# Optimization experiments

Hardware: AMD Instinct MI355X
Metric: run time of the kernel (lower is better)

The kernel has to match this reference:

```python
import jax, jax.numpy as jnp
import numpy as np

B, N, DIN, D, HID, C, K = 16, 1024, 768, 512, 128, 20, 64
H = W = 32
EPS = 1e-5  # BatchNorm eps (inference mode with running stats)


def _conv(x, w, pad=0, dil=1):
    return jax.lax.conv_general_dilated(
        x, w, (1, 1), [(pad, pad), (pad, pad)],
        rhs_dilation=(dil, dil),
        dimension_numbers=('NCHW', 'OIHW', 'NCHW'))


def _bn(x, g, b, m, v):
    inv = jax.lax.rsqrt(v + EPS)
    return (x - m[None, :, None, None]) * (g * inv)[None, :, None, None] + b[None, :, None, None]


def _l2norm(x):
    n = jnp.sqrt(jnp.sum(x * x, axis=-1, keepdims=True))
    return x / jnp.maximum(n, 1e-12)  # matches F.normalize(eps=1e-12)


def setup_inputs():
    key = jax.random.key(0)
    ks = jax.random.split(key, 12)

    def conv_w(k, o, i, kh, kw):
        return jax.random.normal(k, (o, i, kh, kw), jnp.float32) / np.sqrt(i * kh * kw)

    def bn_p(k, c):
        k1, k2 = jax.random.split(k)
        return (jnp.ones(c, jnp.float32), jnp.zeros(c, jnp.float32),
                0.1 * jax.random.normal(k1, (c,), jnp.float32),
                jax.random.uniform(k2, (c,), jnp.float32, 0.5, 1.5))

    g0, b0, m0, v0 = bn_p(ks[3], D)
    gr, br, mr, vr = bn_p(ks[4], HID)
    gl, bl, ml, vl = bn_p(ks[5], HID)
    gg, bg, mg, vg = bn_p(ks[6], HID)
    gp, bp, mp, vp = bn_p(ks[7], D)
    return {
        'patch_feats': jax.random.normal(ks[0], (B, N, DIN), jnp.float32),
        'protos': _l2norm(jax.random.normal(ks[1], (C, K, D), jnp.float32)),  # hybrid protos, L2-normed as in __init__
        'w0': conv_w(ks[2], D, DIN, 1, 1), 'g0': g0, 'b0': b0, 'm0': m0, 'v0': v0,
        'wr': conv_w(ks[8], HID, D, 1, 1), 'gr': gr, 'br': br, 'mr': mr, 'vr': vr,
        'wl': conv_w(ks[9], HID, HID, 3, 3), 'gl': gl, 'bl': bl, 'ml': ml, 'vl': vl,
        'wg': conv_w(ks[10], HID, HID, 3, 3), 'gg': gg, 'bg': bg, 'mg': mg, 'vg': vg,
        'wp': conv_w(ks[11], D, 2 * HID, 1, 1), 'gp': gp, 'bp': bp, 'mp': mp, 'vp': vp,
        'wf': conv_w(jax.random.fold_in(key, 99), D, D, 1, 1),
        'bf': jnp.zeros(D, jnp.float32),
        'logit_scale': jnp.float32(10.0),
    }


def reference(patch_feats, protos, w0, g0, b0, m0, v0, wr, gr, br, mr, vr,
              wl, gl, bl, ml, vl, wg, gg, bg, mg, vg, wp, gp, bp, mp, vp,
              wf, bf, logit_scale):
    Bq, Nq, Din = patch_feats.shape
    x = patch_feats.transpose(0, 2, 1).reshape(Bq, Din, H, W)
    # adapter: 1x1 conv -> BN -> ReLU
    x = jax.nn.relu(_bn(_conv(x, w0), g0, b0, m0, v0))
    # ResidualContextBlock
    res = x
    o = jax.nn.relu(_bn(_conv(x, wr), gr, br, mr, vr))
    l = jax.nn.relu(_bn(_conv(o, wl, pad=1), gl, bl, ml, vl))
    g = jax.nn.relu(_bn(_conv(o, wg, pad=2, dil=2), gg, bg, mg, vg))
    o = _bn(_conv(jnp.concatenate([l, g], axis=1), wp), gp, bp, mp, vp)
    x = jax.nn.relu(o + res)
    # final 1x1 conv (with bias)
    x = _conv(x, wf) + bf[None, :, None, None]
    # back to [B, N, D], L2 normalize
    x = x.reshape(Bq, D, Nq).transpose(0, 2, 1)
    x = _l2norm(x)
    # per-class cosine sims + double max reduction (vectorized over classes)
    sims = jnp.einsum('bnd,ckd->bcnk', x, protos)  # [B,C,N,K]
    A = sims.max(axis=-1)                          # [B,C,N] patch->proto max
    act_maps = A.reshape(Bq, C, H, W)
    logits = A.max(axis=-1) * logit_scale          # [B,C]
    return logits, act_maps, x
```

## Files before the change

kernel.cpp:

```cpp
#include <hip/hip_runtime.h>
#include <math.h>

#define BN_EPS 1e-5f

typedef __attribute__((ext_vector_type(8))) short short8v;
typedef __attribute__((ext_vector_type(8))) unsigned short ushort8v;
typedef __attribute__((ext_vector_type(4))) float f32x4;

__device__ __forceinline__ unsigned short f2b(float f) {
    unsigned int u = __float_as_uint(f);
    return (unsigned short)((u + 0x7FFFu + ((u >> 16) & 1u)) >> 16);
}
__device__ __forceinline__ float b2f(unsigned short h) {
    return __uint_as_float(((unsigned int)h) << 16);
}

__global__ __launch_bounds__(256) void f2b_kernel(
    const float* __restrict__ in, unsigned short* __restrict__ out, int n8)
{
    int i = blockIdx.x * 256 + threadIdx.x;
    if (i >= n8) return;
    const float4* p = (const float4*)(in + (size_t)i * 8);
    float4 a = p[0], b = p[1];
    ushort8v r;
    r[0] = f2b(a.x); r[1] = f2b(a.y); r[2] = f2b(a.z); r[3] = f2b(a.w);
    r[4] = f2b(b.x); r[5] = f2b(b.y); r[6] = f2b(b.z); r[7] = f2b(b.w);
    *(ushort8v*)(out + (size_t)i * 8) = r;
}

__global__ __launch_bounds__(256) void convw_kernel(
    const float* __restrict__ wl, const float* __restrict__ wg,
    unsigned short* __restrict__ out)
{
    int i = blockIdx.x * 256 + threadIdx.x;
    if (i >= 294912) return;
    int br = i >= 147456;
    int j  = i - br * 147456;
    int tap = j >> 14, oc = (j >> 7) & 127, ic = j & 127;
    const float* src = br ? wg : wl;
    out[i] = f2b(src[((oc << 7) + ic) * 9 + tap]);
}

__global__ __launch_bounds__(256) void zero_kernel(unsigned short* __restrict__ p, int n8)
{
    int i = blockIdx.x * 256 + threadIdx.x;
    if (i >= n8) return;
    ushort8v z;
#pragma unroll
    for (int k = 0; k < 8; ++k) z[k] = 0;
    *(ushort8v*)(p + (size_t)i * 8) = z;
}

template <int EPI>
__global__ __launch_bounds__(256) void mfma_gemm(
    const unsigned short* __restrict__ A, int lda,
    const unsigned short* __restrict__ Wt, int ldw,
    void* __restrict__ outp, int ldc, int Kdim,
    const float* __restrict__ bng, const float* __restrict__ bnb,
    const float* __restrict__ bnm, const float* __restrict__ bnv,
    const unsigned short* __restrict__ res, int ldres,
    const float* __restrict__ bias)
{
    __shared__ short8v Asta[512];
    __shared__ short8v Bsta[512];
    const int t  = threadIdx.x;
    const int l  = t & 63, w = t >> 6;
    const int wm = w >> 1, wn = w & 1;
    const int m0 = blockIdx.x << 7, n0 = blockIdx.y << 7;

    const int r0  = t & 127;
    const int kb0 = t >> 7;

    const unsigned short* Ap = A  + (size_t)(m0 + r0) * lda + kb0 * 8;
    const unsigned short* Bp = Wt + (size_t)(n0 + r0) * ldw + kb0 * 8;

    f32x4 acc[4][4];
#pragma unroll
    for (int mf = 0; mf < 4; ++mf)
#pragma unroll
        for (int nf = 0; nf < 4; ++nf)
#pragma unroll
            for (int j = 0; j < 4; ++j) acc[mf][nf][j] = 0.f;

    const int arow = wm * 64 + (l & 15);
    const int brow = wn * 64 + (l & 15);
    const int kq   = l >> 4;

    for (int k0 = 0; k0 < Kdim; k0 += 32) {
        short8v a0 = *(const short8v*)(Ap + k0);
        short8v a1 = *(const short8v*)(Ap + k0 + 16);
        short8v b0 = *(const short8v*)(Bp + k0);
        short8v b1 = *(const short8v*)(Bp + k0 + 16);
        __syncthreads();
        Asta[kb0 * 128 + r0]       = a0;
        Asta[(kb0 + 2) * 128 + r0] = a1;
        Bsta[kb0 * 128 + r0]       = b0;
        Bsta[(kb0 + 2) * 128 + r0] = b1;
        __syncthreads();
        short8v af[4], bfv[4];
#pragma unroll
        for (int mf = 0; mf < 4; ++mf) af[mf]  = Asta[kq * 128 + arow + mf * 16];
#pragma unroll
        for (int nf = 0; nf < 4; ++nf) bfv[nf] = Bsta[kq * 128 + brow + nf * 16];
#pragma unroll
        for (int mf = 0; mf < 4; ++mf)
#pragma unroll
            for (int nf = 0; nf < 4; ++nf)
                acc[mf][nf] = __builtin_amdgcn_mfma_f32_16x16x32_bf16(
                    af[mf], bfv[nf], acc[mf][nf], 0, 0, 0);
    }

    float s[4], sh[4];
    int cols[4];
#pragma unroll
    for (int nf = 0; nf < 4; ++nf) {
        int col = n0 + wn * 64 + nf * 16 + (l & 15);
        cols[nf] = col;
        if (EPI == 2) { s[nf] = 1.f; sh[nf] = bias[col]; }
        else {
            float sc = bng[col] * rsqrtf(bnv[col] + BN_EPS);
            s[nf]  = sc;
            sh[nf] = bnb[col] - bnm[col] * sc;
        }
    }
#pragma unroll
    for (int mf = 0; mf < 4; ++mf) {
#pragma unroll
        for (int j = 0; j < 4; ++j) {
            int row = m0 + wm * 64 + mf * 16 + kq * 4 + j;
#pragma unroll
            for (int nf = 0; nf < 4; ++nf) {
                float v = acc[mf][nf][j] * s[nf] + sh[nf];
                if (EPI == 1) v += b2f(res[(size_t)row * ldres + cols[nf]]);
                if (EPI != 2) v = fmaxf(v, 0.f);
                if (EPI == 2) {
                    ((float*)outp)[(size_t)row * ldc + cols[nf]] = v;
                } else if (EPI == 3) {
                    int b = row >> 10, h = (row >> 5) & 31, ww = row & 31;
                    size_t pidx = ((size_t)(b * 36 + h + 2) * 36 + (ww + 2)) * 128 + cols[nf];
                    ((unsigned short*)outp)[pidx] = f2b(v);
                } else {
                    ((unsigned short*)outp)[(size_t)row * ldc + cols[nf]] = f2b(v);
                }
            }
        }
    }
}

__global__ __launch_bounds__(256) void conv_mfma(
    const unsigned short* __restrict__ opad,
    const unsigned short* __restrict__ wt_all,
    const float* __restrict__ g1, const float* __restrict__ b1,
    const float* __restrict__ m1, const float* __restrict__ v1,
    const float* __restrict__ g2, const float* __restrict__ b2,
    const float* __restrict__ m2, const float* __restrict__ v2,
    unsigned short* __restrict__ lg)
{
    __shared__ short8v Asta[512];
    __shared__ short8v Bsta[512];
    const int t  = threadIdx.x;
    const int l  = t & 63, w = t >> 6;
    const int wm = w >> 1, wn = w & 1;
    const int m0 = blockIdx.x << 7;
    const int br = blockIdx.y;
    const int dil = 1 + br;
    const unsigned short* wtb = wt_all + (size_t)br * 147456;

    const int r0  = t & 127;
    const int kb0 = t >> 7;
    const int m   = m0 + r0;
    const int bb  = m >> 10, h = (m >> 5) & 31, wc = m & 31;
    const ptrdiff_t pbase = ((ptrdiff_t)(bb * 36 + h + 2) * 36 + (wc + 2)) * 128;

    f32x4 acc[4][4];
#pragma unroll
    for (int mf = 0; mf < 4; ++mf)
#pragma unroll
        for (int nf = 0; nf < 4; ++nf)
#pragma unroll
            for (int j = 0; j < 4; ++j) acc[mf][nf][j] = 0.f;

    const int arow = wm * 64 + (l & 15);
    const int brow = wn * 64 + (l & 15);
    const int kq   = l >> 4;

    for (int tap = 0; tap < 9; ++tap) {
        const int dh = tap / 3 - 1, dw = tap % 3 - 1;
        const unsigned short* Ap  = opad + pbase + (ptrdiff_t)((dh * 36 + dw) * dil) * 128 + kb0 * 8;
        const unsigned short* Bpt = wtb + (size_t)tap * 16384 + (size_t)r0 * 128 + kb0 * 8;
#pragma unroll
        for (int k0 = 0; k0 < 128; k0 += 32) {
            short8v a0 = *(const short8v*)(Ap + k0);
            short8v a1 = *(const short8v*)(Ap + k0 + 16);
            short8v b0 = *(const short8v*)(Bpt + k0);
            short8v b1 = *(const short8v*)(Bpt + k0 + 16);
            __syncthreads();
            Asta[kb0 * 128 + r0]       = a0;
            Asta[(kb0 + 2) * 128 + r0] = a1;
            Bsta[kb0 * 128 + r0]       = b0;
            Bsta[(kb0 + 2) * 128 + r0] = b1;
            __syncthreads();
            short8v af[4], bfv[4];
#pragma unroll
            for (int mf = 0; mf < 4; ++mf) af[mf]  = Asta[kq * 128 + arow + mf * 16];
#pragma unroll
            for (int nf = 0; nf < 4; ++nf) bfv[nf] = Bsta[kq * 128 + brow + nf * 16];
#pragma unroll
            for (int mf = 0; mf < 4; ++mf)
#pragma unroll
                for (int nf = 0; nf < 4; ++nf)
                    acc[mf][nf] = __builtin_amdgcn_mfma_f32_16x16x32_bf16(
                        af[mf], bfv[nf], acc[mf][nf], 0, 0, 0);
        }
    }

    const float* gg = br ? g2 : g1;
    const float* gb = br ? b2 : b1;
    const float* gm = br ? m2 : m1;
    const float* gv = br ? v2 : v1;
    float s[4], sh[4];
    int cols[4];
#pragma unroll
    for (int nf = 0; nf < 4; ++nf) {
        int col = wn * 64 + nf * 16 + (l & 15);
        cols[nf] = col;
        float sc = gg[col] * rsqrtf(gv[col] + BN_EPS);
        s[nf]  = sc;
        sh[nf] = gb[col] - gm[col] * sc;
    }
#pragma unroll
    for (int mf = 0; mf < 4; ++mf) {
#pragma unroll
        for (int j = 0; j < 4; ++j) {
            int row = m0 + wm * 64 + mf * 16 + kq * 4 + j;
#pragma unroll
            for (int nf = 0; nf < 4; ++nf) {
                float v = fmaxf(acc[mf][nf][j] * s[nf] + sh[nf], 0.f);
                lg[(size_t)row * 256 + br * 128 + cols[nf]] = f2b(v);
            }
        }
    }
}

__global__ __launch_bounds__(256) void l2norm_rows(
    float* __restrict__ x, unsigned short* __restrict__ xn)
{
    const int t    = threadIdx.x;
    const int wv   = t >> 6, lane = t & 63;
    const int row  = (blockIdx.x << 2) + wv;
    float* p = x + (size_t)row * 512 + (lane << 3);
    float4 a = *(float4*)p;
    float4 b = *(float4*)(p + 4);
    float ss = a.x * a.x + a.y * a.y + a.z * a.z + a.w * a.w +
               b.x * b.x + b.y * b.y + b.z * b.z + b.w * b.w;
#pragma unroll
    for (int off = 32; off >= 1; off >>= 1) ss += __shfl_xor(ss, off);
    float sc = 1.f / fmaxf(sqrtf(ss), 1e-12f);
    a.x *= sc; a.y *= sc; a.z *= sc; a.w *= sc;
    b.x *= sc; b.y *= sc; b.z *= sc; b.w *= sc;
    *(float4*)p       = a;
    *(float4*)(p + 4) = b;
    ushort8v r;
    r[0] = f2b(a.x); r[1] = f2b(a.y); r[2] = f2b(a.z); r[3] = f2b(a.w);
    r[4] = f2b(b.x); r[5] = f2b(b.y); r[6] = f2b(b.z); r[7] = f2b(b.w);
    *(ushort8v*)(xn + (size_t)row * 512 + (lane << 3)) = r;
}

__global__ __launch_bounds__(256) void sims_mfma(
    const unsigned short* __restrict__ xn,
    const unsigned short* __restrict__ protos,
    float* __restrict__ act)
{
    __shared__ short8v Asta[512];
    __shared__ short8v Bsta[256];
    const int t = threadIdx.x;
    const int l = t & 63, w = t >> 6;
    const int m0 = blockIdx.x << 7;
    const int c  = blockIdx.y;

    const int r0  = t & 127, kb0 = t >> 7;
    const int rb  = t & 63,  kbb = t >> 6;
    const unsigned short* Ap = xn + (size_t)(m0 + r0) * 512 + kb0 * 8;
    const unsigned short* Bp = protos + ((size_t)c * 64 + rb) * 512 + kbb * 8;

    f32x4 acc[2][4];
#pragma unroll
    for (int mf = 0; mf < 2; ++mf)
#pragma unroll
        for (int nf = 0; nf < 4; ++nf)
#pragma unroll
            for (int j = 0; j < 4; ++j) acc[mf][nf][j] = 0.f;

    const int arow = w * 32 + (l & 15);
    const int brow = l & 15;
    const int kq   = l >> 4;

    for (int k0 = 0; k0 < 512; k0 += 32) {
        short8v a0 = *(const short8v*)(Ap + k0);
        short8v a1 = *(const short8v*)(Ap + k0 + 16);
        short8v b0 = *(const short8v*)(Bp + k0);
        __syncthreads();
        Asta[kb0 * 128 + r0]       = a0;
        Asta[(kb0 + 2) * 128 + r0] = a1;
        Bsta[kbb * 64 + rb]        = b0;
        __syncthreads();
        short8v af[2], bfv[4];
        af[0] = Asta[kq * 128 + arow];
        af[1] = Asta[kq * 128 + arow + 16];
#pragma unroll
        for (int nf = 0; nf < 4; ++nf) bfv[nf] = Bsta[kq * 64 + brow + nf * 16];
#pragma unroll
        for (int mf = 0; mf < 2; ++mf)
#pragma unroll
            for (int nf = 0; nf < 4; ++nf)
                acc[mf][nf] = __builtin_amdgcn_mfma_f32_16x16x32_bf16(
                    af[mf], bfv[nf], acc[mf][nf], 0, 0, 0);
    }

#pragma unroll
    for (int mf = 0; mf < 2; ++mf) {
        float vj[4];
#pragma unroll
        for (int j = 0; j < 4; ++j) {
            float v = fmaxf(fmaxf(acc[mf][0][j], acc[mf][1][j]),
                            fmaxf(acc[mf][2][j], acc[mf][3][j]));
            v = fmaxf(v, __shfl_xor(v, 1));
            v = fmaxf(v, __shfl_xor(v, 2));
            v = fmaxf(v, __shfl_xor(v, 4));
            v = fmaxf(v, __shfl_xor(v, 8));
            vj[j] = v;
        }
        if ((l & 15) == 0) {
            int rowb = m0 + w * 32 + mf * 16 + kq * 4;
#pragma unroll
            for (int j = 0; j < 4; ++j) {
                int row = rowb + j;
                int bb = row >> 10, n = row & 1023;
                act[(((size_t)(bb * 20 + c)) << 10) + n] = vj[j];
            }
        }
    }
}

__global__ __launch_bounds__(256) void logits_max(
    const float* __restrict__ act, const float* __restrict__ lsc,
    float* __restrict__ logits)
{
    const int bc = blockIdx.x;
    const int t  = threadIdx.x;
    float4 v = *(const float4*)(act + ((size_t)bc << 10) + (t << 2));
    float mx = fmaxf(fmaxf(v.x, v.y), fmaxf(v.z, v.w));
#pragma unroll
    for (int off = 32; off >= 1; off >>= 1) mx = fmaxf(mx, __shfl_xor(mx, off));
    __shared__ float wm[4];
    if ((t & 63) == 0) wm[t >> 6] = mx;
    __syncthreads();
    if (t == 0) {
        float m2 = fmaxf(fmaxf(wm[0], wm[1]), fmaxf(wm[2], wm[3]));
        logits[bc] = m2 * lsc[0];
    }
}

extern "C" void kernel_launch(void* const* d_in, const int* in_sizes, int n_in,
                              void* d_out, int out_size, void* d_ws, size_t ws_size,
                              hipStream_t stream)
{
    const float* pf   = (const float*)d_in[0];
    const float* prot = (const float*)d_in[1];
    const float* w0   = (const float*)d_in[2];
    const float* g0   = (const float*)d_in[3];
    const float* b0   = (const float*)d_in[4];
    const float* m0v  = (const float*)d_in[5];
    const float* v0   = (const float*)d_in[6];
    const float* wr   = (const float*)d_in[7];
    const float* gr   = (const float*)d_in[8];
    const float* br   = (const float*)d_in[9];
    const float* mr   = (const float*)d_in[10];
    const float* vr   = (const float*)d_in[11];
    const float* wl   = (const float*)d_in[12];
    const float* gl   = (const float*)d_in[13];
    const float* bl   = (const float*)d_in[14];
    const float* ml   = (const float*)d_in[15];
    const float* vl   = (const float*)d_in[16];
    const float* wg   = (const float*)d_in[17];
    const float* gG   = (const float*)d_in[18];
    const float* bG   = (const float*)d_in[19];
    const float* mG   = (const float*)d_in[20];
    const float* vG   = (const float*)d_in[21];
    const float* wp   = (const float*)d_in[22];
    const float* gp   = (const float*)d_in[23];
    const float* bp   = (const float*)d_in[24];
    const float* mp   = (const float*)d_in[25];
    const float* vp   = (const float*)d_in[26];
    const float* wf   = (const float*)d_in[27];
    const float* bf_  = (const float*)d_in[28];
    const float* lsc  = (const float*)d_in[29];

    char* ws = (char*)d_ws;
    unsigned short* pf_bf    = (unsigned short*)(ws);
    unsigned short* w0_bf    = (unsigned short*)(ws + 25165824);
    unsigned short* wr_bf    = (unsigned short*)(ws + 25952256);
    unsigned short* wt_bf    = (unsigned short*)(ws + 26083328);
    unsigned short* wp_bf    = (unsigned short*)(ws + 26673152);
    unsigned short* wf_bf    = (unsigned short*)(ws + 26935296);
    unsigned short* prot_bf  = (unsigned short*)(ws + 27459584);
    unsigned short* x1_bf    = (unsigned short*)(ws + 28770304);
    unsigned short* opad     = (unsigned short*)(ws + 45547520);
    unsigned short* lg_bf    = (unsigned short*)(ws + 50855936);
    unsigned short* x2_bf    = (unsigned short*)(ws + 59244544);
    unsigned short* xn_bf    = (unsigned short*)(ws + 76021760);

    float* out    = (float*)d_out;
    float* logits = out;
    float* act    = out + 320;
    float* xo     = out + 328000;

    f2b_kernel<<<6144, 256, 0, stream>>>(pf,   pf_bf,   1572864);
    f2b_kernel<<<192,  256, 0, stream>>>(w0,   w0_bf,   49152);
    f2b_kernel<<<32,   256, 0, stream>>>(wr,   wr_bf,   8192);
    f2b_kernel<<<64,   256, 0, stream>>>(wp,   wp_bf,   16384);
    f2b_kernel<<<128,  256, 0, stream>>>(wf,   wf_bf,   32768);
    f2b_kernel<<<320,  256, 0, stream>>>(prot, prot_bf, 81920);
    convw_kernel<<<1152, 256, 0, stream>>>(wl, wg, wt_bf);
    zero_kernel<<<1296, 256, 0, stream>>>(opad, 331776);

    mfma_gemm<0><<<dim3(128, 4), 256, 0, stream>>>(
        pf_bf, 768, w0_bf, 768, x1_bf, 512, 768,
        g0, b0, m0v, v0, nullptr, 0, nullptr);

    mfma_gemm<3><<<dim3(128, 1), 256, 0, stream>>>(
        x1_bf, 512, wr_bf, 512, opad, 0, 512,
        gr, br, mr, vr, nullptr, 0, nullptr);

    conv_mfma<<<dim3(128, 2), 256, 0, stream>>>(
        opad, wt_bf, gl, bl, ml, vl, gG, bG, mG, vG, lg_bf);

    mfma_gemm<1><<<dim3(128, 4), 256, 0, stream>>>(
        lg_bf, 256, wp_bf, 256, x2_bf, 512, 256,
        gp, bp, mp, vp, x1_bf, 512, nullptr);

    mfma_gemm<2><<<dim3(128, 4), 256, 0, stream>>>(
        x2_bf, 512, wf_bf, 512, xo, 512, 512,
        nullptr, nullptr, nullptr, nullptr, nullptr, 0, bf_);

    l2norm_rows<<<4096, 256, 0, stream>>>(xo, xn_bf);

    sims_mfma<<<dim3(128, 20), 256, 0, stream>>>(xn_bf, prot_bf, act);

    logits_max<<<320, 256, 0, stream>>>(act, lsc, logits);
}
```

Measured before the change: 226.9 us.

## Retile dilated conv and sims kernels, batch weight conversions into one launch

The five small weight fp32-to-bf16 conversion launches are merged into a single kernel that dispatches by index range. The 3x3 conv kernel now uses 64-row tiles and stages a full 128-wide K slice per tap, so there are two barriers per tap instead of eight, and twice as many blocks are launched. The similarity kernel now covers two classes (128 prototypes) per block with a 4x4 MFMA tile per wave, so each loaded activation tile is reused across more prototypes and half as many blocks are launched. The trade-offs are more LDS per conv block and lower occupancy or parallelism in the sims kernel.

```diff
diff --git a/kernel.cpp b/kernel.cpp
--- a/kernel.cpp
+++ b/kernel.cpp
@@ -26,6 +26,30 @@
     r[0] = f2b(a.x); r[1] = f2b(a.y); r[2] = f2b(a.z); r[3] = f2b(a.w);
     r[4] = f2b(b.x); r[5] = f2b(b.y); r[6] = f2b(b.z); r[7] = f2b(b.w);
     *(ushort8v*)(out + (size_t)i * 8) = r;
+}
+
+__global__ __launch_bounds__(256) void f2b_multi(
+    const float* __restrict__ w0, const float* __restrict__ wr,
+    const float* __restrict__ wp, const float* __restrict__ wf,
+    const float* __restrict__ prot,
+    unsigned short* __restrict__ w0o, unsigned short* __restrict__ wro,
+    unsigned short* __restrict__ wpo, unsigned short* __restrict__ wfo,
+    unsigned short* __restrict__ proto)
+{
+    int i = blockIdx.x * 256 + threadIdx.x;
+    const float* src; unsigned short* dst; int off;
+    if      (i <  49152) { src = w0;   dst = w0o;   off = i; }
+    else if (i <  57344) { src = wr;   dst = wro;   off = i - 49152; }
+    else if (i <  73728) { src = wp;   dst = wpo;   off = i - 57344; }
+    else if (i < 106496) { src = wf;   dst = wfo;   off = i - 73728; }
+    else if (i < 188416) { src = prot; dst = proto; off = i - 106496; }
+    else return;
+    const float4* p = (const float4*)(src + (size_t)off * 8);
+    float4 a = p[0], b = p[1];
+    ushort8v r;
+    r[0] = f2b(a.x); r[1] = f2b(a.y); r[2] = f2b(a.z); r[3] = f2b(a.w);
+    r[4] = f2b(b.x); r[5] = f2b(b.y); r[6] = f2b(b.z); r[7] = f2b(b.w);
+    *(ushort8v*)(dst + (size_t)off * 8) = r;
 }
 
 __global__ __launch_bounds__(256) void convw_kernel(
@@ -156,57 +180,59 @@
     const float* __restrict__ m2, const float* __restrict__ v2,
     unsigned short* __restrict__ lg)
 {
-    __shared__ short8v Asta[512];
-    __shared__ short8v Bsta[512];
-    const int t  = threadIdx.x;
-    const int l  = t & 63, w = t >> 6;
+    __shared__ short8v Asta[1024];
+    __shared__ short8v Bsta[2048];
+    const int t = threadIdx.x;
+    const int l = t & 63, w = t >> 6;
     const int wm = w >> 1, wn = w & 1;
-    const int m0 = blockIdx.x << 7;
+    const int m0 = blockIdx.x << 6;
     const int br = blockIdx.y;
     const int dil = 1 + br;
     const unsigned short* wtb = wt_all + (size_t)br * 147456;
 
-    const int r0  = t & 127;
-    const int kb0 = t >> 7;
+    const int r0  = t & 63,  kb0 = t >> 6;
+    const int rb  = t & 127, kbb = t >> 7;
     const int m   = m0 + r0;
     const int bb  = m >> 10, h = (m >> 5) & 31, wc = m & 31;
     const ptrdiff_t pbase = ((ptrdiff_t)(bb * 36 + h + 2) * 36 + (wc + 2)) * 128;
 
-    f32x4 acc[4][4];
-#pragma unroll
-    for (int mf = 0; mf < 4; ++mf)
+    f32x4 acc[2][4];
+#pragma unroll
+    for (int mf = 0; mf < 2; ++mf)
 #pragma unroll
         for (int nf = 0; nf < 4; ++nf)
 #pragma unroll
             for (int j = 0; j < 4; ++j) acc[mf][nf][j] = 0.f;
 
-    const int arow = wm * 64 + (l & 15);
-    const int brow = wn * 64 + (l & 15);
+    const int arow = wm * 32 + (l & 15);
+    const int bcol = wn * 64 + (l & 15);
     const int kq   = l >> 4;
 
     for (int tap = 0; tap < 9; ++tap) {
         const int dh = tap / 3 - 1, dw = tap % 3 - 1;
-        const unsigned short* Ap  = opad + pbase + (ptrdiff_t)((dh * 36 + dw) * dil) * 128 + kb0 * 8;
-        const unsigned short* Bpt = wtb + (size_t)tap * 16384 + (size_t)r0 * 128 + kb0 * 8;
-#pragma unroll
-        for (int k0 = 0; k0 < 128; k0 += 32) {
-            short8v a0 = *(const short8v*)(Ap + k0);
-            short8v a1 = *(const short8v*)(Ap + k0 + 16);
-            short8v b0 = *(const short8v*)(Bpt + k0);
-            short8v b1 = *(const short8v*)(Bpt + k0 + 16);
-            __syncthreads();
-            Asta[kb0 * 128 + r0]       = a0;
-            Asta[(kb0 + 2) * 128 + r0] = a1;
-            Bsta[kb0 * 128 + r0]       = b0;
-            Bsta[(kb0 + 2) * 128 + r0] = b1;
-            __syncthreads();
-            short8v af[4], bfv[4];
-#pragma unroll
-            for (int mf = 0; mf < 4; ++mf) af[mf]  = Asta[kq * 128 + arow + mf * 16];
-#pragma unroll
-            for (int nf = 0; nf < 4; ++nf) bfv[nf] = Bsta[kq * 128 + brow + nf * 16];
-#pragma unroll
-            for (int mf = 0; mf < 4; ++mf)
+        const unsigned short* Ap = opad + pbase + (ptrdiff_t)((dh * 36 + dw) * dil) * 128;
+        const unsigned short* Bp = wtb + (size_t)tap * 16384 + (size_t)rb * 128;
+        short8v av[4], bv[8];
+#pragma unroll
+        for (int i = 0; i < 4; ++i) av[i] = *(const short8v*)(Ap + (kb0 + 4 * i) * 8);
+#pragma unroll
+        for (int i = 0; i < 8; ++i) bv[i] = *(const short8v*)(Bp + (kbb + 2 * i) * 8);
+        __syncthreads();
+#pragma unroll
+        for (int i = 0; i < 4; ++i) Asta[(kb0 + 4 * i) * 64 + r0] = av[i];
+#pragma unroll
+        for (int i = 0; i < 8; ++i) Bsta[(kbb + 2 * i) * 128 + rb] = bv[i];
+        __syncthreads();
+#pragma unroll
+        for (int kk = 0; kk < 4; ++kk) {
+            short8v af[2], bfv[4];
+            af[0] = Asta[(kq + 4 * kk) * 64 + arow];
+            af[1] = Asta[(kq + 4 * kk) * 64 + arow + 16];
+#pragma unroll
+            for (int nf = 0; nf < 4; ++nf)
+                bfv[nf] = Bsta[(kq + 4 * kk) * 128 + bcol + nf * 16];
+#pragma unroll
+            for (int mf = 0; mf < 2; ++mf)
 #pragma unroll
                 for (int nf = 0; nf < 4; ++nf)
                     acc[mf][nf] = __builtin_amdgcn_mfma_f32_16x16x32_bf16(
@@ -222,17 +248,17 @@
     int cols[4];
 #pragma unroll
     for (int nf = 0; nf < 4; ++nf) {
-        int col = wn * 64 + nf * 16 + (l & 15);
+        int col = bcol + nf * 16;
         cols[nf] = col;
         float sc = gg[col] * rsqrtf(gv[col] + BN_EPS);
         s[nf]  = sc;
         sh[nf] = gb[col] - gm[col] * sc;
     }
 #pragma unroll
-    for (int mf = 0; mf < 4; ++mf) {
+    for (int mf = 0; mf < 2; ++mf) {
 #pragma unroll
         for (int j = 0; j < 4; ++j) {
-            int row = m0 + wm * 64 + mf * 16 + kq * 4 + j;
+            int row = m0 + wm * 32 + mf * 16 + kq * 4 + j;
 #pragma unroll
             for (int nf = 0; nf < 4; ++nf) {
                 float v = fmaxf(acc[mf][nf][j] * s[nf] + sh[nf], 0.f);
@@ -272,53 +298,55 @@
     float* __restrict__ act)
 {
     __shared__ short8v Asta[512];
-    __shared__ short8v Bsta[256];
+    __shared__ short8v Bsta[512];
     const int t = threadIdx.x;
     const int l = t & 63, w = t >> 6;
+    const int wm = w >> 1, wn = w & 1;
     const int m0 = blockIdx.x << 7;
-    const int c  = blockIdx.y;
 
     const int r0  = t & 127, kb0 = t >> 7;
-    const int rb  = t & 63,  kbb = t >> 6;
     const unsigned short* Ap = xn + (size_t)(m0 + r0) * 512 + kb0 * 8;
-    const unsigned short* Bp = protos + ((size_t)c * 64 + rb) * 512 + kbb * 8;
-
-    f32x4 acc[2][4];
-#pragma unroll
-    for (int mf = 0; mf < 2; ++mf)
+    const unsigned short* Bp = protos + ((size_t)blockIdx.y * 128 + r0) * 512 + kb0 * 8;
+
+    f32x4 acc[4][4];
+#pragma unroll
+    for (int mf = 0; mf < 4; ++mf)
 #pragma unroll
         for (int nf = 0; nf < 4; ++nf)
 #pragma unroll
             for (int j = 0; j < 4; ++j) acc[mf][nf][j] = 0.f;
 
-    const int arow = w * 32 + (l & 15);
-    const int brow = l & 15;
+    const int arow = wm * 64 + (l & 15);
+    const int brow = wn * 64 + (l & 15);
     const int kq   = l >> 4;
 
     for (int k0 = 0; k0 < 512; k0 += 32) {
         short8v a0 = *(const short8v*)(Ap + k0);
         short8v a1 = *(const short8v*)(Ap + k0 + 16);
         short8v b0 = *(const short8v*)(Bp + k0);
+        short8v b1 = *(const short8v*)(Bp + k0 + 16);
         __syncthreads();
         Asta[kb0 * 128 + r0]       = a0;
         Asta[(kb0 + 2) * 128 + r0] = a1;
-        Bsta[kbb * 64 + rb]        = b0;
-        __syncthreads();
-        short8v af[2], bfv[4];
-        af[0] = Asta[kq * 128 + arow];
-        af[1] = Asta[kq * 128 + arow + 16];
-#pragma unroll
-        for (int nf = 0; nf < 4; ++nf) bfv[nf] = Bsta[kq * 64 + brow + nf * 16];
-#pragma unroll
-        for (int mf = 0; mf < 2; ++mf)
+        Bsta[kb0 * 128 + r0]       = b0;
+        Bsta[(kb0 + 2) * 128 + r0] = b1;
+        __syncthreads();
+        short8v af[4], bfv[4];
+#pragma unroll
+        for (int mf = 0; mf < 4; ++mf) af[mf]  = Asta[kq * 128 + arow + mf * 16];
+#pragma unroll
+        for (int nf = 0; nf < 4; ++nf) bfv[nf] = Bsta[kq * 128 + brow + nf * 16];
+#pragma unroll
+        for (int mf = 0; mf < 4; ++mf)
 #pragma unroll
             for (int nf = 0; nf < 4; ++nf)
                 acc[mf][nf] = __builtin_amdgcn_mfma_f32_16x16x32_bf16(
                     af[mf], bfv[nf], acc[mf][nf], 0, 0, 0);
     }
 
-#pragma unroll
-    for (int mf = 0; mf < 2; ++mf) {
+    const int c = (blockIdx.y << 1) + wn;
+#pragma unroll
+    for (int mf = 0; mf < 4; ++mf) {
         float vj[4];
 #pragma unroll
         for (int j = 0; j < 4; ++j) {
@@ -331,7 +359,7 @@
             vj[j] = v;
         }
         if ((l & 15) == 0) {
-            int rowb = m0 + w * 32 + mf * 16 + kq * 4;
+            int rowb = m0 + wm * 64 + mf * 16 + kq * 4;
 #pragma unroll
             for (int j = 0; j < 4; ++j) {
                 int row = rowb + j;
@@ -415,12 +443,9 @@
     float* act    = out + 320;
     float* xo     = out + 328000;
 
-    f2b_kernel<<<6144, 256, 0, stream>>>(pf,   pf_bf,   1572864);
-    f2b_kernel<<<192,  256, 0, stream>>>(w0,   w0_bf,   49152);
-    f2b_kernel<<<32,   256, 0, stream>>>(wr,   wr_bf,   8192);
-    f2b_kernel<<<64,   256, 0, stream>>>(wp,   wp_bf,   16384);
-    f2b_kernel<<<128,  256, 0, stream>>>(wf,   wf_bf,   32768);
-    f2b_kernel<<<320,  256, 0, stream>>>(prot, prot_bf, 81920);
+    f2b_kernel<<<6144, 256, 0, stream>>>(pf, pf_bf, 1572864);
+    f2b_multi<<<736, 256, 0, stream>>>(w0, wr, wp, wf, prot,
+                                       w0_bf, wr_bf, wp_bf, wf_bf, prot_bf);
     convw_kernel<<<1152, 256, 0, stream>>>(wl, wg, wt_bf);
     zero_kernel<<<1296, 256, 0, stream>>>(opad, 331776);
 
@@ -432,7 +457,7 @@
         x1_bf, 512, wr_bf, 512, opad, 0, 512,
         gr, br, mr, vr, nullptr, 0, nullptr);
 
-    conv_mfma<<<dim3(128, 2), 256, 0, stream>>>(
+    conv_mfma<<<dim3(256, 2), 256, 0, stream>>>(
         opad, wt_bf, gl, bl, ml, vl, gG, bG, mG, vG, lg_bf);
 
     mfma_gemm<1><<<dim3(128, 4), 256, 0, stream>>>(
@@ -445,7 +470,7 @@
 
     l2norm_rows<<<4096, 256, 0, stream>>>(xo, xn_bf);
 
-    sims_mfma<<<dim3(128, 20), 256, 0, stream>>>(xn_bf, prot_bf, act);
+    sims_mfma<<<dim3(128, 10), 256, 0, stream>>>(xn_bf, prot_bf, act);
 
     logits_max<<<320, 256, 0, stream>>>(act, lsc, logits);
 }
```

Measured after the change: 204.1 us. 10.0% less time.
